# Kernel tuning notes

Hardware: AMD Instinct MI355X
Metric: run time of the kernel (lower is better)

Reference implementation:

```python
import jax, jax.numpy as jnp
from jax import lax
import numpy as np

B, V, T, K, HE, TH, E, L = 128, 30000, 50, 50, 256, 800, 300, 3
DELTA = 0.005


def setup_inputs() -> dict:
    key = jax.random.key(0)
    ks = jax.random.split(key, 24)
    rn = lambda k, s, sc=0.05: jax.random.normal(k, s, jnp.float32) * sc
    return dict(
        X=jax.random.uniform(ks[0], (B, V), jnp.float32),
        timestamp=jax.random.randint(ks[1], (B,), 0, T),
        X_mean=jax.random.uniform(ks[2], (T, V), jnp.float32),
        W_eta_map=rn(ks[3], (HE, V)), b_eta_map=rn(ks[4], (HE,)),
        lstm_Wih=rn(ks[5], (L, 4 * HE, HE)), lstm_Whh=rn(ks[6], (L, 4 * HE, HE)),
        lstm_bih=rn(ks[7], (L, 4 * HE)), lstm_bhh=rn(ks[8], (L, 4 * HE)),
        W_qeta_mu=rn(ks[9], (K, HE + K)), b_qeta_mu=rn(ks[10], (K,)),
        W_qeta_ls=rn(ks[11], (K, HE + K)), b_qeta_ls=rn(ks[12], (K,)),
        W1=rn(ks[13], (TH, V + K)), b1=rn(ks[14], (TH,)),
        W2=rn(ks[15], (TH, TH)), b2=rn(ks[16], (TH,)),
        W_qt_mu=rn(ks[17], (K, TH)), b_qt_mu=rn(ks[18], (K,)),
        W_qt_ls=rn(ks[19], (K, TH)), b_qt_ls=rn(ks[20], (K,)),
        mu_q_alpha=rn(ks[21], (K, T, E), 0.1),
        logsigma_q_alpha=rn(ks[22], (K, T, E), 0.1),
        emb=rn(ks[23], (V, E), 0.1),
    )


def _lstm(x, Wih, Whh, bih, bhh):
    # PyTorch-style multi-layer LSTM, batch=1 squeezed away; x: [T, HE]
    for l in range(Wih.shape[0]):
        Wi, Wh, bi, bh = Wih[l], Whh[l], bih[l], bhh[l]
        def step(carry, xt, Wi=Wi, Wh=Wh, bi=bi, bh=bh):
            h, c = carry
            g = Wi @ xt + Wh @ h + bi + bh
            i, f, gg, o = jnp.split(g, 4)  # torch gate order i,f,g,o
            c = jax.nn.sigmoid(f) * c + jax.nn.sigmoid(i) * jnp.tanh(gg)
            h = jax.nn.sigmoid(o) * jnp.tanh(c)
            return (h, c), h
        H = Wh.shape[1]
        _, x = lax.scan(step, (jnp.zeros(H, x.dtype), jnp.zeros(H, x.dtype)), x)
    return x


def reference(X, timestamp, X_mean, W_eta_map, b_eta_map, lstm_Wih, lstm_Whh,
              lstm_bih, lstm_bhh, W_qeta_mu, b_qeta_mu, W_qeta_ls, b_qeta_ls,
              W1, b1, W2, b2, W_qt_mu, b_qt_mu, W_qt_ls, b_qt_ls,
              mu_q_alpha, logsigma_q_alpha, emb):
    # eval-mode DETM forward (reparameterize returns mu when not training)
    nb = X / X.sum(1, keepdims=True)
    logd = jnp.log(jnp.float32(DELTA))
    Tn = X_mean.shape[0]
    first = jnp.arange(Tn) == 0

    # --- eta: LSTM over time then sequential Gaussian recurrence ---
    rnn_out = _lstm(X_mean @ W_eta_map.T + b_eta_map, lstm_Wih, lstm_Whh, lstm_bih, lstm_bhh)  # [T,HE]
    Kn = W_qeta_mu.shape[0]

    def eta_step(eta_prev, xs):
        out_t, f = xs
        h = jnp.concatenate([out_t, eta_prev])
        mu = W_qeta_mu @ h + b_qeta_mu
        ls = W_qeta_ls @ h + b_qeta_ls
        p_ls = jnp.where(f, 0.0, logd)  # prior: N(0,I) at t=0, N(eta_{t-1}, delta) after
        kl = 0.5 * jnp.sum((jnp.exp(ls) + (mu - eta_prev) ** 2) / (jnp.exp(p_ls) + 1e-6) - 1.0 + p_ls - ls)
        return mu, (mu, kl)  # eval: eta_t = mu_t

    _, (etas, kls_eta) = lax.scan(eta_step, jnp.zeros(Kn, X.dtype), (rnn_out, first))
    kl_eta = kls_eta.sum()

    # --- theta ---
    eta_td = etas[timestamp]  # [B,K]
    h = jnp.tanh(jnp.concatenate([nb, eta_td], axis=1) @ W1.T + b1)
    h = jnp.tanh(h @ W2.T + b2)
    mu_t = h @ W_qt_mu.T + b_qt_mu
    ls_t = h @ W_qt_ls.T + b_qt_ls
    theta = jax.nn.softmax(mu_t, axis=-1)  # eval: z = mu
    kl_theta = (0.5 * jnp.sum((jnp.exp(ls_t) + (mu_t - eta_td) ** 2) / (1.0 + 1e-6) - 1.0 - ls_t, axis=-1)).sum()

    # --- alpha (eval: alpha_t = mu_q_alpha[:,t,:]) ---
    alphas = jnp.transpose(mu_q_alpha, (1, 0, 2))      # [T,K,E]
    q_ls = jnp.transpose(logsigma_q_alpha, (1, 0, 2))
    p_mu = jnp.concatenate([jnp.zeros_like(alphas[:1]), alphas[:-1]], axis=0)
    p_ls = jnp.where(first[:, None, None], 0.0, logd)
    kl_alpha = (0.5 * jnp.sum((jnp.exp(q_ls) + (alphas - p_mu) ** 2) / (jnp.exp(p_ls) + 1e-6) - 1.0 + p_ls - q_ls, axis=-1)).sum()

    # --- beta, likelihood ---
    beta = jax.nn.softmax(jnp.einsum('tke,ve->tkv', alphas, emb), axis=-1)  # [T,K,V]
    px = jnp.einsum('bk,bkv->bv', theta, beta[timestamp])
    lnpx = jnp.log(px + 1e-6)
    nll = (-lnpx * X).sum(-1).mean()
    return theta, lnpx, beta, nll, kl_alpha, kl_eta, kl_theta
```

## Files before the change

### kernel.cpp

```cpp
#include <hip/hip_runtime.h>
#include <math.h>

#define B_  128
#define V_  30000
#define T_  50
#define K_  50
#define HE_ 256
#define TH_ 800
#define E_  300
#define L_  3

#define LOGD_ (-5.2983173665480363f)

typedef short bf16x8 __attribute__((ext_vector_type(8)));
typedef float f32x4  __attribute__((ext_vector_type(4)));

#define TM 64
#define TN 64
#define TK 16

__global__ __launch_bounds__(256) void gemm_nt(
    const float* __restrict__ A, int lda, int M,
    const float* __restrict__ B, int ldb, int N,
    int K,
    float* __restrict__ C, int ldc,
    const float* __restrict__ bias, int mode, int kchunk)
{
    __shared__ float As[TK][TM + 4];
    __shared__ float Bs[TK][TN + 4];
    const int tid = threadIdx.x;
    const int bm = blockIdx.y * TM;
    const int bn = blockIdx.x * TN;
    const int tx = tid & 15;
    const int ty = tid >> 4;
    const int lr = tid >> 2;
    const int lc = (tid & 3) << 2;

    float acc[4][4];
#pragma unroll
    for (int i = 0; i < 4; ++i)
#pragma unroll
        for (int j = 0; j < 4; ++j) acc[i][j] = 0.f;

    const int kbeg = blockIdx.z * kchunk;
    const int kend = min(K, kbeg + kchunk);

    for (int k0 = kbeg; k0 < kend; k0 += TK) {
        {
            float v0 = 0.f, v1 = 0.f, v2 = 0.f, v3 = 0.f;
            int gr = bm + lr;
            if (gr < M) {
                const float* p = A + (size_t)gr * lda + k0 + lc;
                int rem = K - (k0 + lc);
                if (rem >= 4) {
                    float2 a0 = *(const float2*)p;
                    float2 a1 = *(const float2*)(p + 2);
                    v0 = a0.x; v1 = a0.y; v2 = a1.x; v3 = a1.y;
                } else {
                    if (rem > 0) v0 = p[0];
                    if (rem > 1) v1 = p[1];
                    if (rem > 2) v2 = p[2];
                }
            }
            As[lc + 0][lr] = v0; As[lc + 1][lr] = v1;
            As[lc + 2][lr] = v2; As[lc + 3][lr] = v3;
        }
        {
            float v0 = 0.f, v1 = 0.f, v2 = 0.f, v3 = 0.f;
            int gr = bn + lr;
            if (gr < N) {
                const float* p = B + (size_t)gr * ldb + k0 + lc;
                int rem = K - (k0 + lc);
                if (rem >= 4) {
                    float2 a0 = *(const float2*)p;
                    float2 a1 = *(const float2*)(p + 2);
                    v0 = a0.x; v1 = a0.y; v2 = a1.x; v3 = a1.y;
                } else {
                    if (rem > 0) v0 = p[0];
                    if (rem > 1) v1 = p[1];
                    if (rem > 2) v2 = p[2];
                }
            }
            Bs[lc + 0][lr] = v0; Bs[lc + 1][lr] = v1;
            Bs[lc + 2][lr] = v2; Bs[lc + 3][lr] = v3;
        }
        __syncthreads();
#pragma unroll
        for (int kk = 0; kk < TK; ++kk) {
            float a[4], b[4];
#pragma unroll
            for (int i = 0; i < 4; ++i) a[i] = As[kk][ty * 4 + i];
#pragma unroll
            for (int j = 0; j < 4; ++j) b[j] = Bs[kk][tx * 4 + j];
#pragma unroll
            for (int i = 0; i < 4; ++i)
#pragma unroll
                for (int j = 0; j < 4; ++j) acc[i][j] += a[i] * b[j];
        }
        __syncthreads();
    }

#pragma unroll
    for (int i = 0; i < 4; ++i) {
        int row = bm + ty * 4 + i;
        if (row >= M) continue;
#pragma unroll
        for (int j = 0; j < 4; ++j) {
            int col = bn + tx * 4 + j;
            if (col >= N) continue;
            float v = acc[i][j];
            if (mode == 3) {
                atomicAdd(&C[(size_t)row * ldc + col], v);
            } else {
                if (mode == 1) v = tanhf(v + bias[col]);
                else if (mode == 2) v = v + bias[col];
                C[(size_t)row * ldc + col] = v;
            }
        }
    }
}

__global__ __launch_bounds__(256) void bias_act(
    float* __restrict__ C, const float* __restrict__ bias,
    int total, int N, int mode)
{
    int idx = blockIdx.x * 256 + threadIdx.x;
    if (idx >= total) return;
    int j = idx % N;
    float v = C[idx] + bias[j];
    if (mode == 1) v = tanhf(v);
    C[idx] = v;
}

__global__ __launch_bounds__(256) void rowsum_inv(const float* __restrict__ X,
                                                  float* __restrict__ inv)
{
    int b = blockIdx.x;
    const float4* p = (const float4*)(X + (size_t)b * V_);
    float s = 0.f;
    for (int i = threadIdx.x; i < V_ / 4; i += 256) {
        float4 v = p[i];
        s += v.x + v.y + v.z + v.w;
    }
    for (int off = 32; off; off >>= 1) s += __shfl_down(s, off);
    __shared__ float red[4];
    int wid = threadIdx.x >> 6, lane = threadIdx.x & 63;
    if (lane == 0) red[wid] = s;
    __syncthreads();
    if (threadIdx.x == 0) inv[b] = 1.f / (red[0] + red[1] + red[2] + red[3]);
}

#define NLB 32

__global__ __launch_bounds__(256) void lstm_all(
    const float* __restrict__ rnn_in,
    const float* __restrict__ Wih,
    const float* __restrict__ Whh,
    const float* __restrict__ bih,
    const float* __restrict__ bhh,
    float* __restrict__ houtA,
    float* __restrict__ houtB,
    float* __restrict__ houtF,
    float* __restrict__ hping,
    int* __restrict__ barcnt)
{
    __shared__ float sx[8 * 36];
    __shared__ float sh[8 * 36];
    __shared__ float sg[32];
    const int tid = threadIdx.x;
    const int blk = blockIdx.x;
    const int row_local = tid >> 3;
    const int chunk = tid & 7;
    const int gate = row_local >> 3;
    const int jloc = row_local & 7;
    const int gr = gate * HE_ + blk * 8 + jloc;
    const int seg = tid >> 5, sidx = tid & 31;

    for (int l = 0; l < L_; ++l) {
        float4 wih[8], whh[8];
        const float4* pi = (const float4*)(Wih + ((size_t)l * 4 * HE_ + gr) * HE_ + chunk * 32);
        const float4* pw = (const float4*)(Whh + ((size_t)l * 4 * HE_ + gr) * HE_ + chunk * 32);
#pragma unroll
        for (int q = 0; q < 8; ++q) { wih[q] = pi[q]; whh[q] = pw[q]; }
        const float bias = bih[l * 4 * HE_ + gr] + bhh[l * 4 * HE_ + gr];
        const float* xs = (l == 0) ? rnn_in : ((l == 1) ? houtA : houtB);
        float* hd = (l == 0) ? houtA : ((l == 1) ? houtB : houtF);
        float cst = 0.f;

        for (int t = 0; t < T_; ++t) {
            const int wb = t & 1, rb = wb ^ 1;
            float xv = xs[t * HE_ + tid];
            float hv = (t > 0) ? hping[rb * HE_ + tid] : 0.f;
            sx[seg * 36 + sidx] = xv;
            sh[seg * 36 + sidx] = hv;
            __syncthreads();

            float acc = 0.f;
#pragma unroll
            for (int q = 0; q < 8; ++q) {
                float4 a = *(const float4*)&sx[chunk * 36 + q * 4];
                float4 b = *(const float4*)&sh[chunk * 36 + q * 4];
                float4 wa = wih[q], wc = whh[q];
                acc += wa.x * a.x + wa.y * a.y + wa.z * a.z + wa.w * a.w
                     + wc.x * b.x + wc.y * b.y + wc.z * b.z + wc.w * b.w;
            }
            acc += __shfl_xor(acc, 1);
            acc += __shfl_xor(acc, 2);
            acc += __shfl_xor(acc, 4);
            if (chunk == 0) sg[row_local] = acc + bias;
            __syncthreads();

            if (tid < 8) {
                float gi = sg[tid], gf = sg[8 + tid], gg = sg[16 + tid], go = sg[24 + tid];
                float si = 1.f / (1.f + expf(-gi));
                float sf = 1.f / (1.f + expf(-gf));
                float so = 1.f / (1.f + expf(-go));
                cst = sf * cst + si * tanhf(gg);
                float hn = so * tanhf(cst);
                int j = blk * 8 + tid;
                hping[wb * HE_ + j] = hn;
                hd[t * HE_ + j] = hn;
            }

            if (tid < 64) __threadfence();
            __syncthreads();
            if (tid == 0) {
                atomicAdd(barcnt, 1);
                const int tgt = (l * T_ + t + 1) * NLB;
                while (atomicAdd(barcnt, 0) < tgt) __builtin_amdgcn_s_sleep(2);
                __threadfence();
            }
            __syncthreads();
        }
    }
}

__global__ __launch_bounds__(256) void eta_scan(
    const float* __restrict__ rnn_out,
    const float* __restrict__ Wmu, const float* __restrict__ bmu,
    const float* __restrict__ Wls, const float* __restrict__ bls,
    float* __restrict__ etas,
    float* __restrict__ kl_eta_out)
{
    __shared__ float hbuf[HE_ + K_];
    __shared__ float smu[K_];
    __shared__ float red[256];
    const int tid = threadIdx.x;
    const int k = tid >> 2, c = tid & 3;
    if (tid < K_) hbuf[HE_ + tid] = 0.f;
    float kl = 0.f;
    __syncthreads();
    for (int t = 0; t < T_; ++t) {
        if (tid < HE_) hbuf[tid] = rnn_out[t * HE_ + tid];
        __syncthreads();
        if (k < K_) {
            const float* wm = Wmu + k * (HE_ + K_);
            const float* wl = Wls + k * (HE_ + K_);
            float am = 0.f, al = 0.f;
            for (int i = c; i < HE_ + K_; i += 4) {
                float hv = hbuf[i];
                am += wm[i] * hv;
                al += wl[i] * hv;
            }
            am += __shfl_xor(am, 1); am += __shfl_xor(am, 2);
            al += __shfl_xor(al, 1); al += __shfl_xor(al, 2);
            if (c == 0) {
                float mu = am + bmu[k];
                float ls = al + bls[k];
                float eprev = hbuf[HE_ + k];
                float pls = (t == 0) ? 0.f : LOGD_;
                float d = mu - eprev;
                kl += 0.5f * ((expf(ls) + d * d) / (expf(pls) + 1e-6f) - 1.f + pls - ls);
                etas[t * K_ + k] = mu;
                smu[k] = mu;
            }
        }
        __syncthreads();
        if (tid < K_) hbuf[HE_ + tid] = smu[tid];
        __syncthreads();
    }
    red[tid] = kl;
    __syncthreads();
    if (tid == 0) {
        float s = 0.f;
        for (int i = 0; i < 256; ++i) s += red[i];
        *kl_eta_out = s;
    }
}

__global__ __launch_bounds__(256) void h1_epilogue(
    const float* __restrict__ C1, const float* __restrict__ inv,
    const float* __restrict__ etas, const int* __restrict__ ts,
    const float* __restrict__ W1, const float* __restrict__ b1,
    float* __restrict__ h1)
{
    int idx = blockIdx.x * 256 + threadIdx.x;
    if (idx >= B_ * TH_) return;
    int b = idx / TH_, j = idx % TH_;
    const float* e = etas + ts[b] * K_;
    const float* w = W1 + (size_t)j * (V_ + K_) + V_;
    float s = 0.f;
#pragma unroll
    for (int k = 0; k < K_; ++k) s += e[k] * w[k];
    h1[idx] = tanhf(C1[idx] * inv[b] + s + b1[j]);
}

__global__ __launch_bounds__(64) void theta_kernel(
    const float* __restrict__ mu_t, const float* __restrict__ ls_t,
    const float* __restrict__ etas, const int* __restrict__ ts,
    float* __restrict__ theta, float* __restrict__ kl_out)
{
    int b = blockIdx.x;
    int lane = threadIdx.x;
    bool ok = lane < K_;
    float m = ok ? mu_t[b * K_ + lane] : -3.4e38f;
    float mx = m;
    for (int off = 32; off; off >>= 1) mx = fmaxf(mx, __shfl_down(mx, off));
    mx = __shfl(mx, 0);
    float e = ok ? expf(m - mx) : 0.f;
    float s = e;
    for (int off = 32; off; off >>= 1) s += __shfl_down(s, off);
    s = __shfl(s, 0);
    if (ok) theta[b * K_ + lane] = e / s;
    float kl = 0.f;
    if (ok) {
        float ls = ls_t[b * K_ + lane];
        float d = m - etas[ts[b] * K_ + lane];
        kl = 0.5f * ((expf(ls) + d * d) / (1.f + 1e-6f) - 1.f - ls);
    }
    for (int off = 32; off; off >>= 1) kl += __shfl_down(kl, off);
    if (lane == 0) atomicAdd(kl_out, kl);
}

#define KP_   320
#define MPAD_ 2560
#define NPAD_ 30080

__global__ __launch_bounds__(256) void conv_alpha(
    const float* __restrict__ mu, short* __restrict__ Ah, short* __restrict__ Al)
{
    int idx = blockIdx.x * 256 + threadIdx.x;
    if (idx >= MPAD_ * KP_) return;
    int row = idx / KP_, e = idx % KP_;
    float v = 0.f;
    if (row < T_ * K_ && e < E_) {
        int t = row / K_, k = row % K_;
        v = mu[((size_t)k * T_ + t) * E_ + e];
    }
    unsigned int u = __float_as_uint(v);
    Ah[idx] = (short)(u >> 16);
    float hf = __uint_as_float(u & 0xFFFF0000u);
    Al[idx] = (short)(__float_as_uint(v - hf) >> 16);
}

__global__ __launch_bounds__(256) void gemm_beta(
    const short* __restrict__ Ah, const short* __restrict__ Al,
    const float* __restrict__ Bf,
    float* __restrict__ Cexp,
    float* __restrict__ bsum)
{
    __shared__ __align__(16) short lds[4 * 8192];
    const int tid = threadIdx.x;
    const int lane = tid & 63;
    const int w = tid >> 6;
    const int wr = w >> 1, wc = w & 1;
    const int bm = blockIdx.y * 128;
    const int bn = blockIdx.x * 128;
    const int l15 = lane & 15, l4 = lane >> 4;

    f32x4 acc[4][4];
#pragma unroll
    for (int mi = 0; mi < 4; ++mi)
#pragma unroll
        for (int ni = 0; ni < 4; ++ni) acc[mi][ni] = (f32x4){0.f, 0.f, 0.f, 0.f};

    for (int k0 = 0; k0 < KP_; k0 += 64) {
#pragma unroll
        for (int q = 0; q < 8; ++q) {
            int L = q * 256 + tid;
            int tile = L >> 10;
            int c = L & 1023;
            int r = c >> 3;
            int k8 = (c & 7) ^ (r & 7);
            const short* src = (tile ? Al : Ah) + (size_t)(bm + r) * KP_ + k0 + k8 * 8;
            *(uint4*)&lds[(size_t)(tile * 1024 + c) * 8] = *(const uint4*)src;
        }
#pragma unroll
        for (int q = 0; q < 4; ++q) {
            int L = q * 256 + tid;
            int r = L >> 3;
            int k8 = (L & 7) ^ (r & 7);
            int rg = bn + r;
            int kb = k0 + k8 * 8;
            float vv[8];
            if (rg < V_ && kb + 8 <= E_) {
                float4 u0 = *(const float4*)(Bf + (size_t)rg * E_ + kb);
                float4 u1 = *(const float4*)(Bf + (size_t)rg * E_ + kb + 4);
                vv[0] = u0.x; vv[1] = u0.y; vv[2] = u0.z; vv[3] = u0.w;
                vv[4] = u1.x; vv[5] = u1.y; vv[6] = u1.z; vv[7] = u1.w;
            } else {
#pragma unroll
                for (int e = 0; e < 8; ++e) {
                    int kk = kb + e;
                    vv[e] = (rg < V_ && kk < E_) ? Bf[(size_t)rg * E_ + kk] : 0.f;
                }
            }
            unsigned int hpk[4], lpk[4];
#pragma unroll
            for (int e = 0; e < 8; e += 2) {
                unsigned int u0 = __float_as_uint(vv[e]);
                unsigned int u1 = __float_as_uint(vv[e + 1]);
                hpk[e >> 1] = (u0 >> 16) | (u1 & 0xFFFF0000u);
                float d0 = vv[e]     - __uint_as_float(u0 & 0xFFFF0000u);
                float d1 = vv[e + 1] - __uint_as_float(u1 & 0xFFFF0000u);
                lpk[e >> 1] = (__float_as_uint(d0) >> 16) | (__float_as_uint(d1) & 0xFFFF0000u);
            }
            uint4 hv; hv.x = hpk[0]; hv.y = hpk[1]; hv.z = hpk[2]; hv.w = hpk[3];
            uint4 lv; lv.x = lpk[0]; lv.y = lpk[1]; lv.z = lpk[2]; lv.w = lpk[3];
            *(uint4*)&lds[(size_t)(2048 + L) * 8] = hv;
            *(uint4*)&lds[(size_t)(3072 + L) * 8] = lv;
        }
        __syncthreads();

#pragma unroll
        for (int ks = 0; ks < 2; ++ks) {
            bf16x8 fah[4], fal[4], fbh[4], fbl[4];
#pragma unroll
            for (int mi = 0; mi < 4; ++mi) {
                int r = wr * 64 + mi * 16 + l15;
                int s = r * 8 + ((ks * 4 + l4) ^ (r & 7));
                fah[mi] = *(const bf16x8*)&lds[(size_t)s * 8];
                fal[mi] = *(const bf16x8*)&lds[(size_t)(1024 + s) * 8];
            }
#pragma unroll
            for (int ni = 0; ni < 4; ++ni) {
                int r = wc * 64 + ni * 16 + l15;
                int s = r * 8 + ((ks * 4 + l4) ^ (r & 7));
                fbh[ni] = *(const bf16x8*)&lds[(size_t)(2048 + s) * 8];
                fbl[ni] = *(const bf16x8*)&lds[(size_t)(3072 + s) * 8];
            }
#pragma unroll
            for (int mi = 0; mi < 4; ++mi)
#pragma unroll
                for (int ni = 0; ni < 4; ++ni) {
                    acc[mi][ni] = __builtin_amdgcn_mfma_f32_16x16x32_bf16(
                        fah[mi], fbh[ni], acc[mi][ni], 0, 0, 0);
                    acc[mi][ni] = __builtin_amdgcn_mfma_f32_16x16x32_bf16(
                        fah[mi], fbl[ni], acc[mi][ni], 0, 0, 0);
                    acc[mi][ni] = __builtin_amdgcn_mfma_f32_16x16x32_bf16(
                        fal[mi], fbh[ni], acc[mi][ni], 0, 0, 0);
                }
        }
        __syncthreads();
    }

#pragma unroll
    for (int mi = 0; mi < 4; ++mi) {
#pragma unroll
        for (int reg = 0; reg < 4; ++reg) {
            int grow = bm + wr * 64 + mi * 16 + (l4 << 2) + reg;
            float rs = 0.f;
            float ex[4];
#pragma unroll
            for (int ni = 0; ni < 4; ++ni) {
                int gcol = bn + wc * 64 + ni * 16 + l15;
                float e = (gcol < V_) ? __expf(acc[mi][ni][reg]) : 0.f;
                ex[ni] = e;
                rs += e;
            }
            if (grow < T_ * K_) {
#pragma unroll
                for (int ni = 0; ni < 4; ++ni) {
                    int gcol = bn + wc * 64 + ni * 16 + l15;
                    if (gcol < V_) Cexp[(size_t)grow * V_ + gcol] = ex[ni];
                }
            }
            rs += __shfl_xor(rs, 1);
            rs += __shfl_xor(rs, 2);
            rs += __shfl_xor(rs, 4);
            rs += __shfl_xor(rs, 8);
            if (l15 == 0 && grow < T_ * K_) atomicAdd(&bsum[grow], rs);
        }
    }
}

__global__ __launch_bounds__(256) void beta_scale(
    float* __restrict__ beta, const float* __restrict__ bsum)
{
    int row = blockIdx.y;
    int c4 = blockIdx.x * 256 + threadIdx.x;
    if (c4 >= V_ / 4) return;
    float inv = 1.f / bsum[row];
    float4* p = (float4*)(beta + (size_t)row * V_) + c4;
    float4 v = *p;
    v.x *= inv; v.y *= inv; v.z *= inv; v.w *= inv;
    *p = v;
}

__global__ __launch_bounds__(256) void px_kernel(
    const float* __restrict__ beta, const float* __restrict__ theta,
    const int* __restrict__ ts, const float* __restrict__ X,
    float* __restrict__ lnpx, float* __restrict__ nll_acc)
{
    __shared__ float sb[K_][256];
    int t = blockIdx.y;
    int tid = threadIdx.x;
    int v = blockIdx.x * 256 + tid;
    bool vok = v < V_;
    bool any = false;
    for (int b = 0; b < B_; ++b) any |= (ts[b] == t);
    if (!any) return;
    for (int k = 0; k < K_; ++k)
        sb[k][tid] = vok ? beta[((size_t)t * K_ + k) * V_ + v] : 0.f;
    __syncthreads();
    float acc = 0.f;
    for (int b = 0; b < B_; ++b) {
        if (ts[b] != t) continue;
        const float* th = theta + b * K_;
        float px = 0.f;
#pragma unroll
        for (int k = 0; k < K_; ++k) px += th[k] * sb[k][tid];
        float l = logf(px + 1e-6f);
        if (vok) {
            lnpx[(size_t)b * V_ + v] = l;
            acc += l * X[(size_t)b * V_ + v];
        }
    }
    for (int off = 32; off; off >>= 1) acc += __shfl_down(acc, off);
    __shared__ float red[4];
    int wid = tid >> 6, lane = tid & 63;
    if (lane == 0) red[wid] = acc;
    __syncthreads();
    if (tid == 0) atomicAdd(nll_acc, red[0] + red[1] + red[2] + red[3]);
}

__global__ __launch_bounds__(256) void kl_alpha_kernel(
    const float* __restrict__ mu, const float* __restrict__ lsig,
    float* __restrict__ out)
{
    int idx = blockIdx.x * 256 + threadIdx.x;
    float term = 0.f;
    if (idx < K_ * T_ * E_) {
        int r = idx % (T_ * E_);
        int t = r / E_;
        float a = mu[idx];
        float q = lsig[idx];
        float pmu = (t > 0) ? mu[idx - E_] : 0.f;
        float pls = (t > 0) ? LOGD_ : 0.f;
        float d = a - pmu;
        term = 0.5f * ((expf(q) + d * d) / (expf(pls) + 1e-6f) - 1.f + pls - q);
    }
    for (int off = 32; off; off >>= 1) term += __shfl_down(term, off);
    __shared__ float red[4];
    int wid = threadIdx.x >> 6, lane = threadIdx.x & 63;
    if (lane == 0) red[wid] = term;
    __syncthreads();
    if (threadIdx.x == 0) atomicAdd(out, red[0] + red[1] + red[2] + red[3]);
}

__global__ void finalize_nll(const float* __restrict__ acc, float* __restrict__ out)
{
    *out = -acc[0] * (1.f / (float)B_);
}

extern "C" void kernel_launch(void* const* d_in, const int* in_sizes, int n_in,
                              void* d_out, int out_size, void* d_ws, size_t ws_size,
                              hipStream_t stream)
{
    const float* X          = (const float*)d_in[0];
    const int*   ts         = (const int*)d_in[1];
    const float* X_mean     = (const float*)d_in[2];
    const float* W_eta_map  = (const float*)d_in[3];
    const float* b_eta_map  = (const float*)d_in[4];
    const float* lstm_Wih   = (const float*)d_in[5];
    const float* lstm_Whh   = (const float*)d_in[6];
    const float* lstm_bih   = (const float*)d_in[7];
    const float* lstm_bhh   = (const float*)d_in[8];
    const float* W_qeta_mu  = (const float*)d_in[9];
    const float* b_qeta_mu  = (const float*)d_in[10];
    const float* W_qeta_ls  = (const float*)d_in[11];
    const float* b_qeta_ls  = (const float*)d_in[12];
    const float* W1         = (const float*)d_in[13];
    const float* b1         = (const float*)d_in[14];
    const float* W2         = (const float*)d_in[15];
    const float* b2         = (const float*)d_in[16];
    const float* W_qt_mu    = (const float*)d_in[17];
    const float* b_qt_mu    = (const float*)d_in[18];
    const float* W_qt_ls    = (const float*)d_in[19];
    const float* b_qt_ls    = (const float*)d_in[20];
    const float* mu_q_alpha = (const float*)d_in[21];
    const float* ls_q_alpha = (const float*)d_in[22];
    const float* emb        = (const float*)d_in[23];

    float* out     = (float*)d_out;
    float* o_theta = out;
    float* o_lnpx  = out + (size_t)B_ * K_;
    float* o_beta  = o_lnpx + (size_t)B_ * V_;
    float* o_scal  = o_beta + (size_t)T_ * K_ * V_;

    float* ws = (float*)d_ws;
    float* w_inv   = ws;
    float* w_rnn   = ws + 128;
    float* w_seq0  = ws + 12928;
    float* w_houtA = ws + 38528;
    float* w_houtB = ws + 51328;
    float* w_hping = ws + 64128;
    float* w_barc  = ws + 64640;
    float* w_etas  = ws + 89728;
    float* w_h1    = ws + 92228;
    float* w_h2    = ws + 194628;
    float* w_mu    = ws + 297028;
    float* w_ls    = ws + 303428;
    float* w_nll   = ws + 309828;
    float* w_bsum  = ws + 309832;
    short* w_Ah    = (short*)(ws + 312344);
    short* w_Al    = (short*)(ws + 721944);

    hipMemsetAsync(o_scal, 0, 4 * sizeof(float), stream);
    hipMemsetAsync(w_h1, 0, (size_t)(102400 + 102400 + 6400 + 6400 + 1) * sizeof(float), stream);
    hipMemsetAsync(w_rnn, 0, (size_t)T_ * HE_ * sizeof(float), stream);
    hipMemsetAsync(w_barc, 0, sizeof(int), stream);
    hipMemsetAsync(w_bsum, 0, (size_t)T_ * K_ * sizeof(float), stream);

    rowsum_inv<<<B_, 256, 0, stream>>>(X, w_inv);

    gemm_nt<<<dim3(HE_ / TN, 1, 125), 256, 0, stream>>>(
        X_mean, V_, T_, W_eta_map, V_, HE_, V_, w_rnn, HE_, nullptr, 3, 240);
    bias_act<<<(T_ * HE_ + 255) / 256, 256, 0, stream>>>(
        w_rnn, b_eta_map, T_ * HE_, HE_, 2);

    lstm_all<<<NLB, 256, 0, stream>>>(
        w_rnn, lstm_Wih, lstm_Whh, lstm_bih, lstm_bhh,
        w_houtA, w_houtB, w_seq0, w_hping, (int*)w_barc);

    eta_scan<<<1, 256, 0, stream>>>(w_seq0, W_qeta_mu, b_qeta_mu,
                                    W_qeta_ls, b_qeta_ls, w_etas, o_scal + 2);

    gemm_nt<<<dim3((TH_ + TN - 1) / TN, (B_ + TM - 1) / TM, 75), 256, 0, stream>>>(
        X, V_, B_, W1, V_ + K_, TH_, V_, w_h1, TH_, nullptr, 3, 400);
    h1_epilogue<<<(B_ * TH_ + 255) / 256, 256, 0, stream>>>(
        w_h1, w_inv, w_etas, ts, W1, b1, w_h1);

    gemm_nt<<<dim3((TH_ + TN - 1) / TN, (B_ + TM - 1) / TM, 10), 256, 0, stream>>>(
        w_h1, TH_, B_, W2, TH_, TH_, TH_, w_h2, TH_, nullptr, 3, 80);
    bias_act<<<(B_ * TH_ + 255) / 256, 256, 0, stream>>>(
        w_h2, b2, B_ * TH_, TH_, 1);

    gemm_nt<<<dim3(1, (B_ + TM - 1) / TM, 25), 256, 0, stream>>>(
        w_h2, TH_, B_, W_qt_mu, TH_, K_, TH_, w_mu, K_, nullptr, 3, 32);
    gemm_nt<<<dim3(1, (B_ + TM - 1) / TM, 25), 256, 0, stream>>>(
        w_h2, TH_, B_, W_qt_ls, TH_, K_, TH_, w_ls, K_, nullptr, 3, 32);
    bias_act<<<(B_ * K_ + 255) / 256, 256, 0, stream>>>(
        w_mu, b_qt_mu, B_ * K_, K_, 2);
    bias_act<<<(B_ * K_ + 255) / 256, 256, 0, stream>>>(
        w_ls, b_qt_ls, B_ * K_, K_, 2);

    theta_kernel<<<B_, 64, 0, stream>>>(w_mu, w_ls, w_etas, ts, o_theta, o_scal + 3);

    conv_alpha<<<(MPAD_ * KP_ + 255) / 256, 256, 0, stream>>>(mu_q_alpha, w_Ah, w_Al);
    gemm_beta<<<dim3(NPAD_ / 128, MPAD_ / 128), 256, 0, stream>>>(
        w_Ah, w_Al, emb, o_beta, w_bsum);
    beta_scale<<<dim3((V_ / 4 + 255) / 256, T_ * K_), 256, 0, stream>>>(o_beta, w_bsum);

    px_kernel<<<dim3((V_ + 255) / 256, T_), 256, 0, stream>>>(
        o_beta, o_theta, ts, X, o_lnpx, w_nll);

    kl_alpha_kernel<<<(K_ * T_ * E_ + 255) / 256, 256, 0, stream>>>(
        mu_q_alpha, ls_q_alpha, o_scal + 1);

    finalize_nll<<<1, 1, 0, stream>>>(w_nll, o_scal);
}
```

Measured before the change: 2.766 ms.

## Pipeline beta GEMM with register prefetch, 512 threads, XCD-aware tile mapping

```diff
diff --git a/kernel.cpp b/kernel.cpp
--- a/kernel.cpp
+++ b/kernel.cpp
@@ -225,10 +225,10 @@
             if (tid < 64) __threadfence();
             __syncthreads();
             if (tid == 0) {
-                atomicAdd(barcnt, 1);
+                __hip_atomic_fetch_add(barcnt, 1, __ATOMIC_ACQ_REL, __HIP_MEMORY_SCOPE_AGENT);
                 const int tgt = (l * T_ + t + 1) * NLB;
-                while (atomicAdd(barcnt, 0) < tgt) __builtin_amdgcn_s_sleep(2);
-                __threadfence();
+                while (__hip_atomic_load(barcnt, __ATOMIC_ACQUIRE, __HIP_MEMORY_SCOPE_AGENT) < tgt)
+                    __builtin_amdgcn_s_sleep(1);
             }
             __syncthreads();
         }
@@ -353,7 +353,7 @@
     Al[idx] = (short)(__float_as_uint(v - hf) >> 16);
 }
 
-__global__ __launch_bounds__(256) void gemm_beta(
+__global__ __launch_bounds__(512, 4) void gemm_beta(
     const short* __restrict__ Ah, const short* __restrict__ Al,
     const float* __restrict__ Bf,
     float* __restrict__ Cexp,
@@ -363,56 +363,85 @@
     const int tid = threadIdx.x;
     const int lane = tid & 63;
     const int w = tid >> 6;
-    const int wr = w >> 1, wc = w & 1;
-    const int bm = blockIdx.y * 128;
-    const int bn = blockIdx.x * 128;
+    const int wr = w >> 2, wc = w & 3;
     const int l15 = lane & 15, l4 = lane >> 4;
 
-    f32x4 acc[4][4];
+    const int NM = MPAD_ / 128;
+    const int nwg = (NPAD_ / 128) * NM;
+    const int qq_ = nwg / 8, rr_ = nwg % 8;
+    int orig = blockIdx.x;
+    int xcd = orig & 7, ixc = orig >> 3;
+    int wg = (xcd < rr_ ? xcd * (qq_ + 1) : rr_ * (qq_ + 1) + (xcd - rr_) * qq_) + ixc;
+    const int bn = (wg / NM) * 128;
+    const int bm = (wg % NM) * 128;
+
+    f32x4 acc[4][2];
 #pragma unroll
     for (int mi = 0; mi < 4; ++mi)
 #pragma unroll
-        for (int ni = 0; ni < 4; ++ni) acc[mi][ni] = (f32x4){0.f, 0.f, 0.f, 0.f};
-
-    for (int k0 = 0; k0 < KP_; k0 += 64) {
-#pragma unroll
-        for (int q = 0; q < 8; ++q) {
-            int L = q * 256 + tid;
+        for (int ni = 0; ni < 2; ++ni) acc[mi][ni] = (f32x4){0.f, 0.f, 0.f, 0.f};
+
+    uint4  va[4];
+    float4 vb[4];
+
+    auto loadTile = [&](int k0) {
+#pragma unroll
+        for (int q = 0; q < 4; ++q) {
+            int L = q * 512 + tid;
             int tile = L >> 10;
             int c = L & 1023;
             int r = c >> 3;
             int k8 = (c & 7) ^ (r & 7);
             const short* src = (tile ? Al : Ah) + (size_t)(bm + r) * KP_ + k0 + k8 * 8;
-            *(uint4*)&lds[(size_t)(tile * 1024 + c) * 8] = *(const uint4*)src;
-        }
-#pragma unroll
-        for (int q = 0; q < 4; ++q) {
-            int L = q * 256 + tid;
+            va[q] = *(const uint4*)src;
+        }
+#pragma unroll
+        for (int q = 0; q < 2; ++q) {
+            int L = q * 512 + tid;
             int r = L >> 3;
             int k8 = (L & 7) ^ (r & 7);
             int rg = bn + r;
             int kb = k0 + k8 * 8;
-            float vv[8];
+            float4 u0, u1;
             if (rg < V_ && kb + 8 <= E_) {
-                float4 u0 = *(const float4*)(Bf + (size_t)rg * E_ + kb);
-                float4 u1 = *(const float4*)(Bf + (size_t)rg * E_ + kb + 4);
-                vv[0] = u0.x; vv[1] = u0.y; vv[2] = u0.z; vv[3] = u0.w;
-                vv[4] = u1.x; vv[5] = u1.y; vv[6] = u1.z; vv[7] = u1.w;
+                u0 = *(const float4*)(Bf + (size_t)rg * E_ + kb);
+                u1 = *(const float4*)(Bf + (size_t)rg * E_ + kb + 4);
             } else {
+                float t[8];
 #pragma unroll
                 for (int e = 0; e < 8; ++e) {
                     int kk = kb + e;
-                    vv[e] = (rg < V_ && kk < E_) ? Bf[(size_t)rg * E_ + kk] : 0.f;
+                    t[e] = (rg < V_ && kk < E_) ? Bf[(size_t)rg * E_ + kk] : 0.f;
                 }
-            }
+                u0.x = t[0]; u0.y = t[1]; u0.z = t[2]; u0.w = t[3];
+                u1.x = t[4]; u1.y = t[5]; u1.z = t[6]; u1.w = t[7];
+            }
+            vb[q * 2] = u0; vb[q * 2 + 1] = u1;
+        }
+    };
+    auto writeTile = [&]() {
+#pragma unroll
+        for (int q = 0; q < 4; ++q) {
+            int L = q * 512 + tid;
+            int tile = L >> 10;
+            int c = L & 1023;
+            *(uint4*)&lds[(size_t)(tile * 1024 + c) * 8] = va[q];
+        }
+#pragma unroll
+        for (int q = 0; q < 2; ++q) {
+            int L = q * 512 + tid;
+            float vv[8];
+            float4 u0 = vb[q * 2], u1 = vb[q * 2 + 1];
+            vv[0] = u0.x; vv[1] = u0.y; vv[2] = u0.z; vv[3] = u0.w;
+            vv[4] = u1.x; vv[5] = u1.y; vv[6] = u1.z; vv[7] = u1.w;
             unsigned int hpk[4], lpk[4];
 #pragma unroll
             for (int e = 0; e < 8; e += 2) {
-                unsigned int u0 = __float_as_uint(vv[e]);
-                unsigned int u1 = __float_as_uint(vv[e + 1]);
-                hpk[e >> 1] = (u0 >> 16) | (u1 & 0xFFFF0000u);
-                float d0 = vv[e]     - __uint_as_float(u0 & 0xFFFF0000u);
-                float d1 = vv[e + 1] - __uint_as_float(u1 & 0xFFFF0000u);
+                unsigned int b0 = __float_as_uint(vv[e]);
+                unsigned int b1 = __float_as_uint(vv[e + 1]);
+                hpk[e >> 1] = (b0 >> 16) | (b1 & 0xFFFF0000u);
+                float d0 = vv[e]     - __uint_as_float(b0 & 0xFFFF0000u);
+                float d1 = vv[e + 1] - __uint_as_float(b1 & 0xFFFF0000u);
                 lpk[e >> 1] = (__float_as_uint(d0) >> 16) | (__float_as_uint(d1) & 0xFFFF0000u);
             }
             uint4 hv; hv.x = hpk[0]; hv.y = hpk[1]; hv.z = hpk[2]; hv.w = hpk[3];
@@ -420,38 +449,48 @@
             *(uint4*)&lds[(size_t)(2048 + L) * 8] = hv;
             *(uint4*)&lds[(size_t)(3072 + L) * 8] = lv;
         }
-        __syncthreads();
+    };
+
+    loadTile(0);
+    writeTile();
+    __syncthreads();
+
+    for (int k0 = 0; k0 < KP_; k0 += 64) {
+        const bool nxt = (k0 + 64) < KP_;
+        if (nxt) loadTile(k0 + 64);
 
 #pragma unroll
         for (int ks = 0; ks < 2; ++ks) {
-            bf16x8 fah[4], fal[4], fbh[4], fbl[4];
+            bf16x8 fbh[2], fbl[2];
+#pragma unroll
+            for (int ni = 0; ni < 2; ++ni) {
+                int r = wc * 32 + ni * 16 + l15;
+                int s = r * 8 + ((ks * 4 + l4) ^ (r & 7));
+                fbh[ni] = *(const bf16x8*)&lds[(size_t)(2048 + s) * 8];
+                fbl[ni] = *(const bf16x8*)&lds[(size_t)(3072 + s) * 8];
+            }
 #pragma unroll
             for (int mi = 0; mi < 4; ++mi) {
                 int r = wr * 64 + mi * 16 + l15;
                 int s = r * 8 + ((ks * 4 + l4) ^ (r & 7));
-                fah[mi] = *(const bf16x8*)&lds[(size_t)s * 8];
-                fal[mi] = *(const bf16x8*)&lds[(size_t)(1024 + s) * 8];
-            }
-#pragma unroll
-            for (int ni = 0; ni < 4; ++ni) {
-                int r = wc * 64 + ni * 16 + l15;
-                int s = r * 8 + ((ks * 4 + l4) ^ (r & 7));
-                fbh[ni] = *(const bf16x8*)&lds[(size_t)(2048 + s) * 8];
-                fbl[ni] = *(const bf16x8*)&lds[(size_t)(3072 + s) * 8];
-            }
-#pragma unroll
-            for (int mi = 0; mi < 4; ++mi)
-#pragma unroll
-                for (int ni = 0; ni < 4; ++ni) {
+                bf16x8 fah = *(const bf16x8*)&lds[(size_t)s * 8];
+                bf16x8 fal = *(const bf16x8*)&lds[(size_t)(1024 + s) * 8];
+#pragma unroll
+                for (int ni = 0; ni < 2; ++ni) {
                     acc[mi][ni] = __builtin_amdgcn_mfma_f32_16x16x32_bf16(
-                        fah[mi], fbh[ni], acc[mi][ni], 0, 0, 0);
+                        fah, fbh[ni], acc[mi][ni], 0, 0, 0);
                     acc[mi][ni] = __builtin_amdgcn_mfma_f32_16x16x32_bf16(
-                        fah[mi], fbl[ni], acc[mi][ni], 0, 0, 0);
+                        fah, fbl[ni], acc[mi][ni], 0, 0, 0);
                     acc[mi][ni] = __builtin_amdgcn_mfma_f32_16x16x32_bf16(
-                        fal[mi], fbh[ni], acc[mi][ni], 0, 0, 0);
+                        fal, fbh[ni], acc[mi][ni], 0, 0, 0);
                 }
+            }
         }
         __syncthreads();
+        if (nxt) {
+            writeTile();
+            __syncthreads();
+        }
     }
 
 #pragma unroll
@@ -460,18 +499,18 @@
         for (int reg = 0; reg < 4; ++reg) {
             int grow = bm + wr * 64 + mi * 16 + (l4 << 2) + reg;
             float rs = 0.f;
-            float ex[4];
-#pragma unroll
-            for (int ni = 0; ni < 4; ++ni) {
-                int gcol = bn + wc * 64 + ni * 16 + l15;
+            float ex[2];
+#pragma unroll
+            for (int ni = 0; ni < 2; ++ni) {
+                int gcol = bn + wc * 32 + ni * 16 + l15;
                 float e = (gcol < V_) ? __expf(acc[mi][ni][reg]) : 0.f;
                 ex[ni] = e;
                 rs += e;
             }
             if (grow < T_ * K_) {
 #pragma unroll
-                for (int ni = 0; ni < 4; ++ni) {
-                    int gcol = bn + wc * 64 + ni * 16 + l15;
+                for (int ni = 0; ni < 2; ++ni) {
+                    int gcol = bn + wc * 32 + ni * 16 + l15;
                     if (gcol < V_) Cexp[(size_t)grow * V_ + gcol] = ex[ni];
                 }
             }
@@ -487,14 +526,14 @@
 __global__ __launch_bounds__(256) void beta_scale(
     float* __restrict__ beta, const float* __restrict__ bsum)
 {
-    int row = blockIdx.y;
-    int c4 = blockIdx.x * 256 + threadIdx.x;
-    if (c4 >= V_ / 4) return;
-    float inv = 1.f / bsum[row];
-    float4* p = (float4*)(beta + (size_t)row * V_) + c4;
-    float4 v = *p;
-    v.x *= inv; v.y *= inv; v.z *= inv; v.w *= inv;
-    *p = v;
+    const int total4 = T_ * K_ * (V_ / 4);
+    for (int i = blockIdx.x * 256 + threadIdx.x; i < total4; i += gridDim.x * 256) {
+        int row = i / (V_ / 4);
+        float inv = 1.f / bsum[row];
+        float4 v = ((const float4*)beta)[i];
+        v.x *= inv; v.y *= inv; v.z *= inv; v.w *= inv;
+        ((float4*)beta)[i] = v;
+    }
 }
 
 __global__ __launch_bounds__(256) void px_kernel(
@@ -658,9 +697,9 @@
     theta_kernel<<<B_, 64, 0, stream>>>(w_mu, w_ls, w_etas, ts, o_theta, o_scal + 3);
 
     conv_alpha<<<(MPAD_ * KP_ + 255) / 256, 256, 0, stream>>>(mu_q_alpha, w_Ah, w_Al);
-    gemm_beta<<<dim3(NPAD_ / 128, MPAD_ / 128), 256, 0, stream>>>(
+    gemm_beta<<<(NPAD_ / 128) * (MPAD_ / 128), 512, 0, stream>>>(
         w_Ah, w_Al, emb, o_beta, w_bsum);
-    beta_scale<<<dim3((V_ / 4 + 255) / 256, T_ * K_), 256, 0, stream>>>(o_beta, w_bsum);
+    beta_scale<<<2048, 256, 0, stream>>>(o_beta, w_bsum);
 
     px_kernel<<<dim3((V_ + 255) / 256, T_), 256, 0, stream>>>(
         o_beta, o_theta, ts, X, o_lnpx, w_nll);
```

Measured after the change: 2.572 ms. 1.08x faster.
